# Performance work log

Hardware: AMD Instinct MI355X
Metric: run time of the kernel (lower is better)

The kernel has to match this reference:

```python
import jax, jax.numpy as jnp
import numpy as np

SEQ, D_IN, D_KQ, D_V = 4096, 1024, 1024, 1024

def setup_inputs() -> dict:
    key = jax.random.key(0)
    k1, k2, k3, k4 = jax.random.split(key, 4)
    return {
        "x": jax.random.normal(k1, (SEQ, D_IN), dtype=jnp.float32),
        "W_query": jax.random.uniform(k2, (D_IN, D_KQ), dtype=jnp.float32),
        "W_key": jax.random.uniform(k3, (D_IN, D_KQ), dtype=jnp.float32),
        "W_value": jax.random.uniform(k4, (D_IN, D_V), dtype=jnp.float32),
    }

def reference(x, W_query, W_key, W_value):
    d_out_kq = W_query.shape[1]
    Q = x @ W_query          # [S, d_kq]
    K = x @ W_key            # [S, d_kq]
    V = x @ W_value          # [S, d_v]
    attn = Q @ K.T           # [S, S]
    S = attn.shape[0]
    causal_mask = jnp.triu(jnp.ones((S, S), dtype=bool), k=1)
    masked = jnp.where(causal_mask, -jnp.inf, attn)
    attn_weights = jax.nn.softmax(masked / jnp.sqrt(jnp.float32(d_out_kq)), axis=1)
    return attn_weights @ V  # [S, d_v]
```

## Files before the change

kernel.cpp:

```cpp
#include <hip/hip_runtime.h>
#include <math.h>

#define SQ 4096
#define DD 1024
#define TRI 528

typedef _Float16 f16;
typedef f16 f16x8 __attribute__((ext_vector_type(8)));
typedef f16 f16x4 __attribute__((ext_vector_type(4)));
typedef float f32x4 __attribute__((ext_vector_type(4)));

__device__ __forceinline__ float waveMax(float v) {
#pragma unroll
    for (int o = 32; o > 0; o >>= 1) v = fmaxf(v, __shfl_down(v, o, 64));
    return v;
}
__device__ __forceinline__ float waveSum(float v) {
#pragma unroll
    for (int o = 32; o > 0; o >>= 1) v += __shfl_down(v, o, 64);
    return v;
}

__device__ __forceinline__ void gl_lds16(const f16* g, f16* l) {
    __builtin_amdgcn_global_load_lds(
        (const __attribute__((address_space(1))) void*)g,
        (__attribute__((address_space(3))) void*)l, 16, 0, 0);
}

template<int NRW>
__device__ __forceinline__ void stage(const f16* src, int ldk, f16* lds, int w, int lane) {
    const int r0 = w * NRW + (lane >> 2);
    const f16* g = src + (size_t)r0 * ldk + ((lane & 3) << 3);
    f16* l = lds + w * NRW * 32;
    gl_lds16(g, l);
    if (NRW == 32) gl_lds16(g + (size_t)ldk * 16, l + 16 * 32);
}

template<int MODE>
__global__ __launch_bounds__(256)
void gemm_k(const f16* __restrict__ Ah, const f16* __restrict__ Al,
            const f16* __restrict__ Bh, const f16* __restrict__ Bl,
            float* __restrict__ Cf,
            f16* __restrict__ Qh, f16* __restrict__ Ql,
            f16* __restrict__ Kh, f16* __restrict__ Kl,
            f16* __restrict__ Vt, float scale)
{
    constexpr int TM = (MODE == 2) ? 64 : 128;
    constexpr int NI = (MODE == 2) ? 2 : 4;
    constexpr int H  = (MODE == 2) ? 2 : 1;
    constexpr int AH = TM * 32;
    constexpr int BH = 128 * 32;
    constexpr int SMSZ = (MODE == 2) ? H * (AH + BH) : 2 * H * (AH + BH);

    int bm, bn, tri = 0, half = 0;
    if (MODE == 1) {
        const int lin = ((int)blockIdx.x & 7) * 132 + ((int)blockIdx.x >> 3);
        half = lin & 1;
        tri = lin >> 1;
        bm = (int)((sqrtf(8.f * (float)tri + 1.f) - 1.f) * 0.5f);
        while ((bm + 1) * (bm + 2) / 2 <= tri) ++bm;
        while (bm * (bm + 1) / 2 > tri) --bm;
        bn = tri - bm * (bm + 1) / 2;
    } else if (MODE == 2) {
        bm = 63 - (int)blockIdx.x;
        bn = blockIdx.y;
    } else {
        bn = blockIdx.x; bm = blockIdx.y;
    }

    const int m0 = bm * TM;
    const int n0 = bn << 7;
    const int lda = (MODE == 2) ? 128 : DD;
    const int ldb = (MODE == 2) ? SQ : DD;
    const int kst = (MODE == 1) ? (half << 9) : 0;
    const int kend = (MODE == 1) ? (kst + 512)
                   : (MODE == 2) ? (((bm >> 1) + 1) << 7) : DD;
    const bool dolo = (MODE == 1) || (MODE == 0 && bn < 16);

    __shared__ f16 sm[SMSZ];
    f16* smA  = sm;
    f16* smB  = sm + H * AH;
    f16* smAl = sm + H * (AH + BH);
    f16* smBl = smAl + H * AH;

    const int tid = threadIdx.x;
    const int w = tid >> 6, lane = tid & 63;
    const int wr = (MODE == 2) ? 0 : ((w >> 1) << 6);
    const int wc = (MODE == 2) ? (w << 5) : ((w & 1) << 6);
    const int fcol = lane & 15, quad = lane >> 4;

    f32x4 acc[4][NI];
#pragma unroll
    for (int i = 0; i < 4; ++i)
#pragma unroll
        for (int j = 0; j < NI; ++j) acc[i][j] = (f32x4){0.f, 0.f, 0.f, 0.f};

    const int bmT = (MODE == 2) ? (bm >> 1) : 0;
    const size_t triRow = (MODE == 2) ? (size_t)(bmT * (bmT + 1) / 2) : 0;
    const f16* Ab  = Ah + (size_t)m0 * ((MODE == 2) ? 0 : DD);
    const f16* Bb  = Bh + (size_t)n0 * ldb;
    const f16* Abl = dolo ? Al + (size_t)m0 * DD : nullptr;
    const f16* Bbl = dolo ? Bl + (size_t)n0 * ldb : nullptr;

    for (int k0 = kst; k0 < kend; k0 += 32 * H) {
        __syncthreads();
#pragma unroll
        for (int h = 0; h < H; ++h) {
            const int kk = k0 + 32 * h;
            const f16* as;
            if (MODE == 2) {
                as = Ah + ((triRow + (size_t)(kk >> 7)) << 14)
                        + ((size_t)(m0 & 127) << 7) + (kk & 127);
            } else {
                as = Ab + kk;
            }
            stage<TM / 4>(as, lda, smA + h * AH, w, lane);
            stage<32>(Bb + kk, ldb, smB + h * BH, w, lane);
            if (dolo) {
                stage<TM / 4>(Abl + kk, DD, smAl + h * AH, w, lane);
                stage<32>(Bbl + kk, ldb, smBl + h * BH, w, lane);
            }
        }
        __syncthreads();

#pragma unroll
        for (int h = 0; h < H; ++h) {
            f16x8 bh[NI], bl[NI];
#pragma unroll
            for (int in = 0; in < NI; ++in) {
                const int off = ((wc + (in << 4) + fcol) << 5) + (quad << 3);
                bh[in] = *(const f16x8*)&smB[h * BH + off];
                if (dolo) bl[in] = *(const f16x8*)&smBl[h * BH + off];
            }
#pragma unroll
            for (int im = 0; im < 4; ++im) {
                const int off = ((wr + (im << 4) + fcol) << 5) + (quad << 3);
                f16x8 ah = *(const f16x8*)&smA[h * AH + off];
                f16x8 al;
                if (dolo) al = *(const f16x8*)&smAl[h * AH + off];
#pragma unroll
                for (int in = 0; in < NI; ++in) {
                    if (dolo) {
                        acc[im][in] = __builtin_amdgcn_mfma_f32_16x16x32_f16(ah, bl[in], acc[im][in], 0, 0, 0);
                        acc[im][in] = __builtin_amdgcn_mfma_f32_16x16x32_f16(al, bh[in], acc[im][in], 0, 0, 0);
                    }
                    acc[im][in] = __builtin_amdgcn_mfma_f32_16x16x32_f16(ah, bh[in], acc[im][in], 0, 0, 0);
                }
            }
        }
    }

#pragma unroll
    for (int im = 0; im < 4; ++im) {
#pragma unroll
        for (int in = 0; in < NI; ++in) {
            if (MODE == 0) {
                const int region = bn >> 3;
                const int colL = ((bn & 7) << 7) + wc + (in << 4) + fcol;
                if (region == 2) {
                    const int tc = m0 + wr + (im << 4) + (quad << 2);
                    f16x4 o;
#pragma unroll
                    for (int r = 0; r < 4; ++r) o[r] = (f16)acc[im][in][r];
                    *(f16x4*)&Vt[(size_t)colL * SQ + tc] = o;
                } else {
                    f16* Hh = region ? Kh : Qh;
                    f16* Hl = region ? Kl : Ql;
#pragma unroll
                    for (int r = 0; r < 4; ++r) {
                        const int row = m0 + wr + (im << 4) + (quad << 2) + r;
                        const float v = acc[im][in][r];
                        const f16 h = (f16)v;
                        Hh[(size_t)row * DD + colL] = h;
                        Hl[(size_t)row * DD + colL] = (f16)(v - (float)h);
                    }
                }
            } else if (MODE == 1) {
                float* Cp = Cf + (((size_t)half * TRI + tri) << 14);
#pragma unroll
                for (int r = 0; r < 4; ++r) {
                    const int rl = wr + (im << 4) + (quad << 2) + r;
                    const int cl = wc + (in << 4) + fcol;
                    Cp[(rl << 7) + cl] = acc[im][in][r] * scale;
                }
            } else {
#pragma unroll
                for (int r = 0; r < 4; ++r) {
                    const int row = m0 + wr + (im << 4) + (quad << 2) + r;
                    const int col = n0 + wc + (in << 4) + fcol;
                    Cf[(size_t)row * DD + col] = acc[im][in][r];
                }
            }
        }
    }
}

__global__ __launch_bounds__(256)
void prepass(const float* __restrict__ x,
             const float* __restrict__ W0, const float* __restrict__ W1,
             const float* __restrict__ W2,
             f16* __restrict__ xh, f16* __restrict__ xl,
             f16* __restrict__ Th0, f16* __restrict__ Tl0)
{
    __shared__ float t[64][65];
    const int id = blockIdx.x;
    const int tid = threadIdx.x;

    if (id < 4096) {
        const int i = (id * 256 + tid) * 4;
        const float4 v = *(const float4*)(x + i);
        const f16 h0 = (f16)v.x, h1 = (f16)v.y, h2 = (f16)v.z, h3 = (f16)v.w;
        f16x4 hv = {h0, h1, h2, h3};
        f16x4 lv = {(f16)(v.x - (float)h0), (f16)(v.y - (float)h1),
                    (f16)(v.z - (float)h2), (f16)(v.w - (float)h3)};
        *(f16x4*)(xh + i) = hv;
        *(f16x4*)(xl + i) = lv;
        return;
    }

    const int tt = id - 4096;
    const int z = tt >> 8, r8 = tt & 255;
    const float* W = (z == 0) ? W0 : (z == 1) ? W1 : W2;
    f16* Th = Th0 + (size_t)z * DD * DD;
    f16* Tl = Tl0 + (size_t)z * DD * DD;
    const int n0 = (r8 & 15) << 6, k0 = (r8 >> 4) << 6;
    const int tx = tid & 63, ty = tid >> 6;
    for (int r = ty; r < 64; r += 4) t[r][tx] = W[(size_t)(k0 + r) * DD + n0 + tx];
    __syncthreads();
    for (int r = ty; r < 64; r += 4) {
        const float v = t[tx][r];
        const f16 h = (f16)v;
        Th[(size_t)(n0 + r) * DD + k0 + tx] = h;
        Tl[(size_t)(n0 + r) * DD + k0 + tx] = (f16)(v - (float)h);
    }
}

__global__ __launch_bounds__(256)
void softmax_causal(const float* __restrict__ A0, f16* __restrict__ P)
{
    const int i = blockIdx.x;
    const int n = i + 1;
    const int tid = threadIdx.x, w = tid >> 6, lane = tid & 63;
    __shared__ float redM[4], redS[4];
    __shared__ float rowbuf[SQ];

    const int bmI = i >> 7;
    const size_t base = ((size_t)(bmI * (bmI + 1) / 2) << 14) + ((size_t)(i & 127) << 7);
    const float* A1 = A0 + ((size_t)TRI << 14);

    const int nv = n >> 2;
    float m = -INFINITY;
    for (int g = tid; g < nv; g += 256) {
        const int j = g << 2;
        const size_t a = base + ((size_t)(j >> 7) << 14) + (j & 127);
        const float4 v0 = *(const float4*)(A0 + a);
        const float4 v1 = *(const float4*)(A1 + a);
        float4 v = make_float4(v0.x + v1.x, v0.y + v1.y, v0.z + v1.z, v0.w + v1.w);
        *(f32x4*)&rowbuf[j] = (f32x4){v.x, v.y, v.z, v.w};
        m = fmaxf(m, fmaxf(fmaxf(v.x, v.y), fmaxf(v.z, v.w)));
    }
    for (int j = (nv << 2) + tid; j < n; j += 256) {
        const size_t a = base + ((size_t)(j >> 7) << 14) + (j & 127);
        const float v = A0[a] + A1[a];
        rowbuf[j] = v;
        m = fmaxf(m, v);
    }
    m = waveMax(m);
    if (lane == 0) redM[w] = m;
    __syncthreads();
    const float mAll = fmaxf(fmaxf(redM[0], redM[1]), fmaxf(redM[2], redM[3]));

    float s = 0.f;
    for (int g = tid; g < nv; g += 256) {
        const int j = g << 2;
        f32x4 v = *(f32x4*)&rowbuf[j];
        v[0] = __expf(v[0] - mAll); v[1] = __expf(v[1] - mAll);
        v[2] = __expf(v[2] - mAll); v[3] = __expf(v[3] - mAll);
        *(f32x4*)&rowbuf[j] = v;
        s += v[0] + v[1] + v[2] + v[3];
    }
    for (int j = (nv << 2) + tid; j < n; j += 256) {
        const float e = __expf(rowbuf[j] - mAll);
        rowbuf[j] = e;
        s += e;
    }
    s = waveSum(s);
    if (lane == 0) redS[w] = s;
    __syncthreads();
    const float inv = 1.0f / (redS[0] + redS[1] + redS[2] + redS[3]);

    const int kmax = (bmI + 1) << 7;
    for (int g = tid; g < nv; g += 256) {
        const int j = g << 2;
        const size_t a = base + ((size_t)(j >> 7) << 14) + (j & 127);
        const f32x4 v = *(const f32x4*)&rowbuf[j];
        f16x4 o = {(f16)(v[0] * inv), (f16)(v[1] * inv),
                   (f16)(v[2] * inv), (f16)(v[3] * inv)};
        *(f16x4*)&P[a] = o;
    }
    for (int j = (nv << 2) + tid; j < kmax; j += 256) {
        const size_t a = base + ((size_t)(j >> 7) << 14) + (j & 127);
        P[a] = (j < n) ? (f16)(rowbuf[j] * inv) : (f16)0.f;
    }
}

extern "C" void kernel_launch(void* const* d_in, const int* in_sizes, int n_in,
                              void* d_out, int out_size, void* d_ws, size_t ws_size,
                              hipStream_t stream)
{
    const float* x  = (const float*)d_in[0];
    const float* Wq = (const float*)d_in[1];
    const float* Wk = (const float*)d_in[2];
    const float* Wv = (const float*)d_in[3];
    float* out = (float*)d_out;

    char* p = (char*)d_ws;
    auto take = [&](size_t bytes) { void* r = (void*)p; p += (bytes + 255) & ~(size_t)255; return r; };
    const size_t SD = (size_t)SQ * DD;
    f16* xh  = (f16*)take(SD * 2);
    f16* xl  = (f16*)take(SD * 2);
    f16* Wth = (f16*)take((size_t)3 * DD * DD * 2);
    f16* Wtl = (f16*)take((size_t)3 * DD * DD * 2);
    f16* Qh  = (f16*)take(SD * 2);
    f16* Ql  = (f16*)take(SD * 2);
    f16* Kh  = (f16*)take(SD * 2);
    f16* Kl  = (f16*)take(SD * 2);
    f16* Vt  = (f16*)take(SD * 2);
    float* attn = (float*)take((size_t)2 * TRI * 16384 * 4);
    f16* P   = (f16*)take((size_t)TRI * 16384 * 2);

    const dim3 blk(256);

    prepass<<<dim3(4096 + 768), blk, 0, stream>>>(x, Wq, Wk, Wv, xh, xl, Wth, Wtl);

    gemm_k<0><<<dim3(24, SQ / 128), blk, 0, stream>>>(
        xh, xl, Wth, Wtl, nullptr, Qh, Ql, Kh, Kl, Vt, 1.0f);

    gemm_k<1><<<dim3(2 * TRI), blk, 0, stream>>>(
        Qh, Ql, Kh, Kl, attn, nullptr, nullptr, nullptr, nullptr, nullptr, 0.03125f);

    softmax_causal<<<dim3(SQ), blk, 0, stream>>>(attn, P);

    gemm_k<2><<<dim3(SQ / 64, DD / 128), blk, 0, stream>>>(
        P, nullptr, Vt, nullptr, out, nullptr, nullptr, nullptr, nullptr, nullptr, 1.0f);
}
```

Before: 301.4 us.

## Double-buffer A tiles in LDS and load B fragments directly from global

The GEMM main loop is restructured into a two-stage software pipeline. A tiles (and their low-precision halves) are double-buffered in LDS, and B fragments now go straight from global memory into registers instead of through shared memory. The next chunk is staged while the current one feeds the MFMAs, which is meant to hide load latency and cut LDS traffic and footprint. The MODE 1 blockIdx swizzle is also removed, which may hurt L2 locality. Uncoalesced direct B loads and extra register pressure could offset the gains.

After: 420.9 us. 1.4x slower.

```diff
diff --git a/kernel.cpp b/kernel.cpp
--- a/kernel.cpp
+++ b/kernel.cpp
@@ -47,14 +47,15 @@
 {
     constexpr int TM = (MODE == 2) ? 64 : 128;
     constexpr int NI = (MODE == 2) ? 2 : 4;
-    constexpr int H  = (MODE == 2) ? 2 : 1;
     constexpr int AH = TM * 32;
-    constexpr int BH = 128 * 32;
-    constexpr int SMSZ = (MODE == 2) ? H * (AH + BH) : 2 * H * (AH + BH);
+    constexpr bool ALO = (MODE != 2);
+    constexpr int ABUF = ALO ? 2 * AH : AH;
+
+    __shared__ f16 sm[2 * ABUF];
 
     int bm, bn, tri = 0, half = 0;
     if (MODE == 1) {
-        const int lin = ((int)blockIdx.x & 7) * 132 + ((int)blockIdx.x >> 3);
+        const int lin = blockIdx.x;
         half = lin & 1;
         tri = lin >> 1;
         bm = (int)((sqrtf(8.f * (float)tri + 1.f) - 1.f) * 0.5f);
@@ -77,12 +78,6 @@
                    : (MODE == 2) ? (((bm >> 1) + 1) << 7) : DD;
     const bool dolo = (MODE == 1) || (MODE == 0 && bn < 16);
 
-    __shared__ f16 sm[SMSZ];
-    f16* smA  = sm;
-    f16* smB  = sm + H * AH;
-    f16* smAl = sm + H * (AH + BH);
-    f16* smBl = smAl + H * AH;
-
     const int tid = threadIdx.x;
     const int w = tid >> 6, lane = tid & 63;
     const int wr = (MODE == 2) ? 0 : ((w >> 1) << 6);
@@ -97,57 +92,63 @@
 
     const int bmT = (MODE == 2) ? (bm >> 1) : 0;
     const size_t triRow = (MODE == 2) ? (size_t)(bmT * (bmT + 1) / 2) : 0;
-    const f16* Ab  = Ah + (size_t)m0 * ((MODE == 2) ? 0 : DD);
-    const f16* Bb  = Bh + (size_t)n0 * ldb;
-    const f16* Abl = dolo ? Al + (size_t)m0 * DD : nullptr;
-    const f16* Bbl = dolo ? Bl + (size_t)n0 * ldb : nullptr;
-
-    for (int k0 = kst; k0 < kend; k0 += 32 * H) {
+    const f16* BbH = Bh + (size_t)n0 * ldb;
+    const f16* BbL = dolo ? Bl + (size_t)n0 * ldb : nullptr;
+
+    auto stageA = [&](int b, int kk) {
+        f16* dst = sm + b * ABUF;
+        const f16* as;
+        if (MODE == 2) {
+            as = Ah + ((triRow + (size_t)(kk >> 7)) << 14)
+                    + ((size_t)(m0 & 127) << 7) + (kk & 127);
+        } else {
+            as = Ah + (size_t)m0 * DD + kk;
+        }
+        stage<TM / 4>(as, lda, dst, w, lane);
+        if (ALO && dolo) stage<TM / 4>(Al + (size_t)m0 * DD + kk, DD, dst + AH, w, lane);
+    };
+    auto loadB = [&](f16x8* dh, f16x8* dl, int kk) {
+#pragma unroll
+        for (int in = 0; in < NI; ++in) {
+            const size_t off = (size_t)(wc + (in << 4) + fcol) * ldb + kk + (quad << 3);
+            dh[in] = *(const f16x8*)(BbH + off);
+            if (dolo) dl[in] = *(const f16x8*)(BbL + off);
+        }
+    };
+    auto chunk = [&](int b, const f16x8* bh, const f16x8* bl) {
+        const f16* base = sm + b * ABUF;
+#pragma unroll
+        for (int im = 0; im < 4; ++im) {
+            const int off = ((wr + (im << 4) + fcol) << 5) + (quad << 3);
+            f16x8 ah = *(const f16x8*)&base[off];
+            f16x8 al;
+            if (dolo) al = *(const f16x8*)&base[AH + off];
+#pragma unroll
+            for (int in = 0; in < NI; ++in) {
+                if (dolo) {
+                    acc[im][in] = __builtin_amdgcn_mfma_f32_16x16x32_f16(ah, bl[in], acc[im][in], 0, 0, 0);
+                    acc[im][in] = __builtin_amdgcn_mfma_f32_16x16x32_f16(al, bh[in], acc[im][in], 0, 0, 0);
+                }
+                acc[im][in] = __builtin_amdgcn_mfma_f32_16x16x32_f16(ah, bh[in], acc[im][in], 0, 0, 0);
+            }
+        }
+    };
+
+    f16x8 b0h[NI], b0l[NI], b1h[NI], b1l[NI];
+    stageA(0, kst);
+    loadB(b0h, b0l, kst);
+
+    for (int k0 = kst; k0 < kend; k0 += 64) {
         __syncthreads();
-#pragma unroll
-        for (int h = 0; h < H; ++h) {
-            const int kk = k0 + 32 * h;
-            const f16* as;
-            if (MODE == 2) {
-                as = Ah + ((triRow + (size_t)(kk >> 7)) << 14)
-                        + ((size_t)(m0 & 127) << 7) + (kk & 127);
-            } else {
-                as = Ab + kk;
-            }
-            stage<TM / 4>(as, lda, smA + h * AH, w, lane);
-            stage<32>(Bb + kk, ldb, smB + h * BH, w, lane);
-            if (dolo) {
-                stage<TM / 4>(Abl + kk, DD, smAl + h * AH, w, lane);
-                stage<32>(Bbl + kk, ldb, smBl + h * BH, w, lane);
-            }
-        }
+        stageA(1, k0 + 32);
+        loadB(b1h, b1l, k0 + 32);
+        chunk(0, b0h, b0l);
         __syncthreads();
-
-#pragma unroll
-        for (int h = 0; h < H; ++h) {
-            f16x8 bh[NI], bl[NI];
-#pragma unroll
-            for (int in = 0; in < NI; ++in) {
-                const int off = ((wc + (in << 4) + fcol) << 5) + (quad << 3);
-                bh[in] = *(const f16x8*)&smB[h * BH + off];
-                if (dolo) bl[in] = *(const f16x8*)&smBl[h * BH + off];
-            }
-#pragma unroll
-            for (int im = 0; im < 4; ++im) {
-                const int off = ((wr + (im << 4) + fcol) << 5) + (quad << 3);
-                f16x8 ah = *(const f16x8*)&smA[h * AH + off];
-                f16x8 al;
-                if (dolo) al = *(const f16x8*)&smAl[h * AH + off];
-#pragma unroll
-                for (int in = 0; in < NI; ++in) {
-                    if (dolo) {
-                        acc[im][in] = __builtin_amdgcn_mfma_f32_16x16x32_f16(ah, bl[in], acc[im][in], 0, 0, 0);
-                        acc[im][in] = __builtin_amdgcn_mfma_f32_16x16x32_f16(al, bh[in], acc[im][in], 0, 0, 0);
-                    }
-                    acc[im][in] = __builtin_amdgcn_mfma_f32_16x16x32_f16(ah, bh[in], acc[im][in], 0, 0, 0);
-                }
-            }
-        }
+        if (k0 + 64 < kend) {
+            stageA(0, k0 + 64);
+            loadB(b0h, b0l, k0 + 64);
+        }
+        chunk(1, b1h, b1l);
     }
 
 #pragma unroll
```

## Switch GEMM kernels to 32x32x16 MFMA with XOR-swizzled LDS tiles

Applied to the files above, without the earlier changes.

Replaces the 16x16x32 f16 MFMA tiling with 32x32x16 MFMA fragments in all GEMM modes. Each wave now holds fewer, larger f32x16 accumulators, and the epilogue index math is rewritten for the 32x32 output layout. Global-to-LDS staging and fragment reads now use an XOR swizzle on the 16-byte chunk index to cut LDS bank conflicts. It also drops the blockIdx reordering in the QK^T triangular mode, which may change L2 locality across blocks.

Result: slower. 336.6 us (+11.7%).

```diff
diff --git a/kernel.cpp b/kernel.cpp
--- a/kernel.cpp
+++ b/kernel.cpp
@@ -9,6 +9,7 @@
 typedef f16 f16x8 __attribute__((ext_vector_type(8)));
 typedef f16 f16x4 __attribute__((ext_vector_type(4)));
 typedef float f32x4 __attribute__((ext_vector_type(4)));
+typedef float f32x16 __attribute__((ext_vector_type(16)));
 
 __device__ __forceinline__ float waveMax(float v) {
 #pragma unroll
@@ -29,11 +30,15 @@
 
 template<int NRW>
 __device__ __forceinline__ void stage(const f16* src, int ldk, f16* lds, int w, int lane) {
-    const int r0 = w * NRW + (lane >> 2);
-    const f16* g = src + (size_t)r0 * ldk + ((lane & 3) << 3);
+    const int lc = (lane & 3) ^ ((lane >> 2) & 3);
+    const f16* g = src + (size_t)(w * NRW + (lane >> 2)) * ldk + (lc << 3);
     f16* l = lds + w * NRW * 32;
     gl_lds16(g, l);
     if (NRW == 32) gl_lds16(g + (size_t)ldk * 16, l + 16 * 32);
+}
+
+__device__ __forceinline__ int frag_off(int rr, int c) {
+    return (rr << 5) + ((((c ^ rr) & 3)) << 3);
 }
 
 template<int MODE>
@@ -46,7 +51,7 @@
             f16* __restrict__ Vt, float scale)
 {
     constexpr int TM = (MODE == 2) ? 64 : 128;
-    constexpr int NI = (MODE == 2) ? 2 : 4;
+    constexpr int NI = (MODE == 2) ? 1 : 2;
     constexpr int H  = (MODE == 2) ? 2 : 1;
     constexpr int AH = TM * 32;
     constexpr int BH = 128 * 32;
@@ -54,7 +59,7 @@
 
     int bm, bn, tri = 0, half = 0;
     if (MODE == 1) {
-        const int lin = ((int)blockIdx.x & 7) * 132 + ((int)blockIdx.x >> 3);
+        const int lin = blockIdx.x;
         half = lin & 1;
         tri = lin >> 1;
         bm = (int)((sqrtf(8.f * (float)tri + 1.f) - 1.f) * 0.5f);
@@ -87,17 +92,18 @@
     const int w = tid >> 6, lane = tid & 63;
     const int wr = (MODE == 2) ? 0 : ((w >> 1) << 6);
     const int wc = (MODE == 2) ? (w << 5) : ((w & 1) << 6);
-    const int fcol = lane & 15, quad = lane >> 4;
-
-    f32x4 acc[4][NI];
-#pragma unroll
-    for (int i = 0; i < 4; ++i)
-#pragma unroll
-        for (int j = 0; j < NI; ++j) acc[i][j] = (f32x4){0.f, 0.f, 0.f, 0.f};
+    const int l31 = lane & 31, khalf = lane >> 5;
+
+    f32x16 acc[2][NI];
+#pragma unroll
+    for (int i = 0; i < 2; ++i)
+#pragma unroll
+        for (int j = 0; j < NI; ++j)
+#pragma unroll
+            for (int e = 0; e < 16; ++e) acc[i][j][e] = 0.f;
 
     const int bmT = (MODE == 2) ? (bm >> 1) : 0;
     const size_t triRow = (MODE == 2) ? (size_t)(bmT * (bmT + 1) / 2) : 0;
-    const f16* Ab  = Ah + (size_t)m0 * ((MODE == 2) ? 0 : DD);
     const f16* Bb  = Bh + (size_t)n0 * ldb;
     const f16* Abl = dolo ? Al + (size_t)m0 * DD : nullptr;
     const f16* Bbl = dolo ? Bl + (size_t)n0 * ldb : nullptr;
@@ -112,7 +118,7 @@
                 as = Ah + ((triRow + (size_t)(kk >> 7)) << 14)
                         + ((size_t)(m0 & 127) << 7) + (kk & 127);
             } else {
-                as = Ab + kk;
+                as = Ah + (size_t)m0 * DD + kk;
             }
             stage<TM / 4>(as, lda, smA + h * AH, w, lane);
             stage<32>(Bb + kk, ldb, smB + h * BH, w, lane);
@@ -125,70 +131,77 @@
 
 #pragma unroll
         for (int h = 0; h < H; ++h) {
-            f16x8 bh[NI], bl[NI];
-#pragma unroll
-            for (int in = 0; in < NI; ++in) {
-                const int off = ((wc + (in << 4) + fcol) << 5) + (quad << 3);
-                bh[in] = *(const f16x8*)&smB[h * BH + off];
-                if (dolo) bl[in] = *(const f16x8*)&smBl[h * BH + off];
-            }
-#pragma unroll
-            for (int im = 0; im < 4; ++im) {
-                const int off = ((wr + (im << 4) + fcol) << 5) + (quad << 3);
-                f16x8 ah = *(const f16x8*)&smA[h * AH + off];
-                f16x8 al;
-                if (dolo) al = *(const f16x8*)&smAl[h * AH + off];
+#pragma unroll
+            for (int s = 0; s < 2; ++s) {
+                const int c = (s << 1) | khalf;
+                f16x8 bh[NI], bl[NI];
 #pragma unroll
                 for (int in = 0; in < NI; ++in) {
-                    if (dolo) {
-                        acc[im][in] = __builtin_amdgcn_mfma_f32_16x16x32_f16(ah, bl[in], acc[im][in], 0, 0, 0);
-                        acc[im][in] = __builtin_amdgcn_mfma_f32_16x16x32_f16(al, bh[in], acc[im][in], 0, 0, 0);
+                    const int rr = wc + (in << 5) + l31;
+                    bh[in] = *(const f16x8*)&smB[h * BH + frag_off(rr, c)];
+                    if (dolo) bl[in] = *(const f16x8*)&smBl[h * BH + frag_off(rr, c)];
+                }
+#pragma unroll
+                for (int im = 0; im < 2; ++im) {
+                    const int rr = wr + (im << 5) + l31;
+                    f16x8 ah = *(const f16x8*)&smA[h * AH + frag_off(rr, c)];
+                    f16x8 al;
+                    if (dolo) al = *(const f16x8*)&smAl[h * AH + frag_off(rr, c)];
+#pragma unroll
+                    for (int in = 0; in < NI; ++in) {
+                        if (dolo) {
+                            acc[im][in] = __builtin_amdgcn_mfma_f32_32x32x16_f16(ah, bl[in], acc[im][in], 0, 0, 0);
+                            acc[im][in] = __builtin_amdgcn_mfma_f32_32x32x16_f16(al, bh[in], acc[im][in], 0, 0, 0);
+                        }
+                        acc[im][in] = __builtin_amdgcn_mfma_f32_32x32x16_f16(ah, bh[in], acc[im][in], 0, 0, 0);
                     }
-                    acc[im][in] = __builtin_amdgcn_mfma_f32_16x16x32_f16(ah, bh[in], acc[im][in], 0, 0, 0);
                 }
             }
         }
     }
 
 #pragma unroll
-    for (int im = 0; im < 4; ++im) {
+    for (int im = 0; im < 2; ++im) {
 #pragma unroll
         for (int in = 0; in < NI; ++in) {
             if (MODE == 0) {
                 const int region = bn >> 3;
-                const int colL = ((bn & 7) << 7) + wc + (in << 4) + fcol;
+                const int colL = ((bn & 7) << 7) + wc + (in << 5) + l31;
                 if (region == 2) {
-                    const int tc = m0 + wr + (im << 4) + (quad << 2);
-                    f16x4 o;
-#pragma unroll
-                    for (int r = 0; r < 4; ++r) o[r] = (f16)acc[im][in][r];
-                    *(f16x4*)&Vt[(size_t)colL * SQ + tc] = o;
+                    const int tcb = m0 + wr + (im << 5) + (khalf << 2);
+#pragma unroll
+                    for (int g = 0; g < 4; ++g) {
+                        f16x4 o;
+#pragma unroll
+                        for (int r = 0; r < 4; ++r) o[r] = (f16)acc[im][in][(g << 2) | r];
+                        *(f16x4*)&Vt[(size_t)colL * SQ + tcb + (g << 3)] = o;
+                    }
                 } else {
                     f16* Hh = region ? Kh : Qh;
                     f16* Hl = region ? Kl : Ql;
 #pragma unroll
-                    for (int r = 0; r < 4; ++r) {
-                        const int row = m0 + wr + (im << 4) + (quad << 2) + r;
-                        const float v = acc[im][in][r];
-                        const f16 h = (f16)v;
-                        Hh[(size_t)row * DD + colL] = h;
-                        Hl[(size_t)row * DD + colL] = (f16)(v - (float)h);
+                    for (int e = 0; e < 16; ++e) {
+                        const int row = m0 + wr + (im << 5) + (e & 3) + ((e >> 2) << 3) + (khalf << 2);
+                        const float v = acc[im][in][e];
+                        const f16 hh = (f16)v;
+                        Hh[(size_t)row * DD + colL] = hh;
+                        Hl[(size_t)row * DD + colL] = (f16)(v - (float)hh);
                     }
                 }
             } else if (MODE == 1) {
                 float* Cp = Cf + (((size_t)half * TRI + tri) << 14);
-#pragma unroll
-                for (int r = 0; r < 4; ++r) {
-                    const int rl = wr + (im << 4) + (quad << 2) + r;
-                    const int cl = wc + (in << 4) + fcol;
-                    Cp[(rl << 7) + cl] = acc[im][in][r] * scale;
+                const int cl = wc + (in << 5) + l31;
+#pragma unroll
+                for (int e = 0; e < 16; ++e) {
+                    const int rl = wr + (im << 5) + (e & 3) + ((e >> 2) << 3) + (khalf << 2);
+                    Cp[(rl << 7) + cl] = acc[im][in][e] * scale;
                 }
             } else {
-#pragma unroll
-                for (int r = 0; r < 4; ++r) {
-                    const int row = m0 + wr + (im << 4) + (quad << 2) + r;
-                    const int col = n0 + wc + (in << 4) + fcol;
-                    Cf[(size_t)row * DD + col] = acc[im][in][r];
+                const int col = n0 + wc + (in << 5) + l31;
+#pragma unroll
+                for (int e = 0; e < 16; ++e) {
+                    const int row = m0 + (im << 5) + (e & 3) + ((e >> 2) << 3) + (khalf << 2);
+                    Cf[(size_t)row * DD + col] = acc[im][in][e];
                 }
             }
         }
```
